# Performance work log

Hardware: AMD Instinct MI355X
Metric: run time of the kernel (lower is better)

## Reference

```python
import math
import jax, jax.numpy as jnp
import numpy as np

FS = 16000          # sample rate implied by undefined global `fs` in source
NFFT = 320          # win_len == frame_len
HOP = 160           # inc
C_SOUND = 340.0
ARRAY_DIS = 0.027


def _steering(F, n_ch, angle_deg):
    # h = conj(exp(-1j*2*pi*f_k * sensor * d * sin(theta)/c)) -> exp(+1j*...)
    f_k = np.arange(F) * (FS // NFFT)                      # integer bins * 50 Hz
    delay = np.arange(n_ch) * ARRAY_DIS * np.sin(angle_deg * np.pi / 180.0) / C_SOUND
    h = np.exp(1j * 2.0 * np.pi * f_k[:, None] * delay[None, :]).astype(np.complex64)
    return jnp.asarray(h)[..., None]                       # [F, C, 1]


def _stft(x, window):
    # x: [B, C, L] float32; torch.stft defaults: center=True, reflect pad
    pad = NFFT // 2
    xp = jnp.pad(x, ((0, 0), (0, 0), (pad, pad)), mode='reflect')
    T = 1 + (xp.shape[-1] - NFFT) // HOP
    idx = jnp.arange(T)[:, None] * HOP + jnp.arange(NFFT)[None, :]
    frames = xp[:, :, idx] * window                        # [B, C, T, NFFT]
    return jnp.fft.rfft(frames, axis=-1)                   # [B, C, T, F] complex64


def _istft(S):
    # S: [B, F, T] complex; torch.istft with default (rectangular) window
    frames = jnp.fft.irfft(jnp.moveaxis(S, 1, 2), n=NFFT, axis=-1)  # [B, T, NFFT]
    B, T, _ = frames.shape
    out_len = NFFT + HOP * (T - 1)
    idx = jnp.arange(T)[:, None] * HOP + jnp.arange(NFFT)[None, :]
    out = jnp.zeros((B, out_len), frames.dtype).at[:, idx].add(frames)
    wsum = jnp.zeros((out_len,), frames.dtype).at[idx.reshape(-1)].add(1.0)
    pad = NFFT // 2
    return (out / wsum)[:, pad:-pad]


def setup_inputs() -> dict:
    key = jax.random.key(0)
    B, L, C = 8, 160000, 4
    mc_wav = jax.random.normal(key, (B, L, C), dtype=jnp.float32)
    # torch.kaiser_window(320, periodic=True, beta=6)
    window = jnp.asarray(np.kaiser(NFFT + 1, 6.0)[:NFFT].astype(np.float32))
    return {"mc_wav": mc_wav, "window": window}


def reference(mc_wav, window):
    B, L, C = mc_wav.shape
    # pre-normalize: remove DC per channel, scale by per-batch global max-abs
    x = mc_wav - jnp.mean(mc_wav, axis=1, keepdims=True)
    x = x / jnp.max(jnp.abs(x), axis=(1, 2), keepdims=True)
    x = jnp.transpose(x, (0, 2, 1))                        # [B, C, L]

    S = _stft(x, window)                                   # [B, C, T, F]
    F = S.shape[-1]
    Xs = jnp.transpose(S, (2, 0, 3, 1))                    # [T, B, F, C] frames-first
    T = Xs.shape[0]

    h1 = _steering(F, C, -40.0)                            # [F, C, 1]
    h2 = _steering(F, C, 40.0)
    eye = jnp.eye(C, dtype=S.dtype)

    def beam(invR, h, X):
        num = jnp.einsum('bfcd,fdo->bfco', invR, h)        # invR @ h  [B,F,C,1]
        den = jnp.einsum('fco,bfco->bf', h.conj(), num)    # h^H invR h
        w = num[..., 0] / den[..., None]                   # [B, F, C]
        return jnp.einsum('bfc,bfc->bf', w.conj(), X)      # w^H X

    def step(RXX, inp):
        X, first = inp                                     # X: [B, F, C]
        outer = jnp.einsum('bfc,bfd->bfcd', X, X.conj())
        RXX = jnp.where(first, outer, 0.05 * RXX + 0.95 * outer)
        tr = jnp.trace(RXX, axis1=-2, axis2=-1)[..., None, None]
        invR = jnp.linalg.inv(RXX + (tr / C) * eye)        # diag-loaded inverse
        return RXX, (beam(invR, h1, X), beam(invR, h2, X))

    RXX0 = jnp.zeros((B, F, C, C), dtype=S.dtype)
    firsts = jnp.arange(T) == 0
    _, (s1, s2) = jax.lax.scan(step, RXX0, (Xs, firsts))

    S1 = jnp.transpose(s1, (1, 2, 0))                      # [B, F, T]
    S2 = jnp.transpose(s2, (1, 2, 0))
    return _istft(S1), _istft(S2)
```

## Files before the change

### kernel.cpp

```cpp
#include <hip/hip_runtime.h>
#include <hip/hip_bf16.h>
#include <math.h>

#define BB 8
#define LL 160000
#define CC 4
#define NFFT 320
#define HOP 160
#define FB 161
#define TT 1001
#define TP 1024
#define RBLK 128
#define PI_D 3.14159265358979323846
#define NPAD 160320

#define SCH 504
#define KWARM 4

#define GM 16016
#define KSEC 352
#define LDK 704
#define KT 11

typedef __attribute__((ext_vector_type(8))) short bf16x8;
typedef __attribute__((ext_vector_type(4))) float f32x4;

__device__ __forceinline__ void ldsdma16(const short* g, short* l){
    __builtin_amdgcn_global_load_lds((const __attribute__((address_space(1))) void*)g,
                                     (__attribute__((address_space(3))) void*)l, 16, 0, 0);
}

__device__ __forceinline__ float2 cmulf(float2 a, float2 b){
    return make_float2(a.x*b.x - a.y*b.y, a.x*b.y + a.y*b.x);
}
__device__ __forceinline__ float2 cmulcj(float2 a, float2 b){
    return make_float2(a.x*b.x + a.y*b.y, a.y*b.x - a.x*b.y);
}
__device__ __forceinline__ float2 cjmul(float2 a, float2 b){
    return make_float2(a.x*b.x + a.y*b.y, a.x*b.y - a.y*b.x);
}
__device__ __forceinline__ float2 csub(float2 a, float2 b){ return make_float2(a.x-b.x, a.y-b.y); }
__device__ __forceinline__ float2 cscale(float2 a, float s){ return make_float2(a.x*s, a.y*s); }
__device__ __forceinline__ float2 cdivf(float2 a, float2 b){
    float inv = 1.0f/(b.x*b.x + b.y*b.y);
    return make_float2((a.x*b.x + a.y*b.y)*inv, (a.y*b.x - a.x*b.y)*inv);
}
__device__ __forceinline__ short bf_hi(float v){
    __hip_bfloat16 h = __float2bfloat16(v);
    short s; __builtin_memcpy(&s, &h, 2); return s;
}
__device__ __forceinline__ short bf_lo(float v){
    __hip_bfloat16 h = __float2bfloat16(v);
    float r = v - __bfloat162float(h);
    __hip_bfloat16 l = __float2bfloat16(r);
    short s; __builtin_memcpy(&s, &l, 2); return s;
}

__global__ void k_gen(const float* __restrict__ win, float* __restrict__ htab,
                      short* __restrict__ Bts, short* __restrict__ Bt){
    int gid = blockIdx.x*256 + threadIdx.x;
    if (gid < 2*FB*CC){
        int i = gid;
        int c = i & 3;
        int k = (i >> 2) % FB;
        int m = i / (FB*CC);
        double coef = 2.0*PI_D*50.0*0.027*sin(40.0*PI_D/180.0)/340.0;
        double sgn = (m == 0) ? -1.0 : 1.0;
        double ph = sgn*coef*(double)k*(double)c;
        double s, c2;
        sincos(ph, &s, &c2);
        ((float2*)htab)[i] = make_float2((float)c2, (float)s);
        return;
    }
    gid -= 2*FB*CC;
    if (gid < 384*640){
        int col = gid / 640, kk = gid % 640;
        int n = (kk >= 320) ? kk - 320 : kk;
        int sec = (kk >= 320) ? 1 : 0;
        float v = 0.f;
        if (col < 2*FB){
            int k = col >> 1;
            double th = 2.0*PI_D*(double)k*(double)n/320.0;
            double s, co; sincos(th, &s, &co);
            double tw = (col & 1) ? -s : co;
            v = (float)((double)win[n]*tw);
        }
        Bts[gid] = sec ? bf_lo(v) : bf_hi(v);
        return;
    }
    gid -= 384*640;
    if (gid < NFFT*LDK){
        int n = gid / LDK, kk = gid % LDK;
        int sec = (kk >= KSEC) ? 1 : 0;
        int kk2 = kk - (sec ? KSEC : 0);
        float v = 0.f;
        if (kk2 < 2*FB){
            int bin = kk2 >> 1;
            double c = ((bin == 0 || bin == 160) ? 1.0 : 2.0) / 320.0;
            double th = 2.0*PI_D*(double)bin*(double)n/320.0;
            double s, co; sincos(th, &s, &co);
            v = (float)((kk2 & 1) ? -c*s : c*co);
        }
        Bt[(size_t)n*LDK + kk] = sec ? bf_lo(v) : bf_hi(v);
    }
}

__global__ __launch_bounds__(256) void k_stats1(const float* __restrict__ in, float* __restrict__ part){
    __shared__ float4 s4[256];
    __shared__ float4 mn4[256];
    __shared__ float4 mx4[256];
    int b = blockIdx.x / RBLK, chunk = blockIdx.x % RBLK;
    int tid = threadIdx.x;
    const float4* p = (const float4*)(in + (size_t)b*LL*CC);
    const int per = LL / RBLK;
    int start = chunk*per;
    float4 s  = make_float4(0.f,0.f,0.f,0.f);
    float4 mn = make_float4( 3.4e38f, 3.4e38f, 3.4e38f, 3.4e38f);
    float4 mx = make_float4(-3.4e38f,-3.4e38f,-3.4e38f,-3.4e38f);
    for (int i = start + tid; i < start + per; i += 256){
        float4 v = p[i];
        s.x += v.x; s.y += v.y; s.z += v.z; s.w += v.w;
        mn.x = fminf(mn.x, v.x); mn.y = fminf(mn.y, v.y); mn.z = fminf(mn.z, v.z); mn.w = fminf(mn.w, v.w);
        mx.x = fmaxf(mx.x, v.x); mx.y = fmaxf(mx.y, v.y); mx.z = fmaxf(mx.z, v.z); mx.w = fmaxf(mx.w, v.w);
    }
    s4[tid] = s; mn4[tid] = mn; mx4[tid] = mx;
    __syncthreads();
    for (int st = 128; st >= 1; st >>= 1){
        if (tid < st){
            float4 a = s4[tid], c = s4[tid+st];
            s4[tid] = make_float4(a.x+c.x, a.y+c.y, a.z+c.z, a.w+c.w);
            float4 d = mn4[tid], e = mn4[tid+st];
            mn4[tid] = make_float4(fminf(d.x,e.x), fminf(d.y,e.y), fminf(d.z,e.z), fminf(d.w,e.w));
            float4 f = mx4[tid], g = mx4[tid+st];
            mx4[tid] = make_float4(fmaxf(f.x,g.x), fmaxf(f.y,g.y), fmaxf(f.z,g.z), fmaxf(f.w,g.w));
        }
        __syncthreads();
    }
    if (tid == 0){
        float* dst = part + (size_t)(b*RBLK + chunk)*12;
        float4 a = s4[0], d = mn4[0], f = mx4[0];
        dst[0]=a.x; dst[1]=a.y; dst[2]=a.z; dst[3]=a.w;
        dst[4]=d.x; dst[5]=d.y; dst[6]=d.z; dst[7]=d.w;
        dst[8]=f.x; dst[9]=f.y; dst[10]=f.z; dst[11]=f.w;
    }
}

__global__ __launch_bounds__(128) void k_stats2(const float* __restrict__ part,
                                                float* __restrict__ mean, float* __restrict__ invmax){
    __shared__ float4 s4[128];
    __shared__ float4 mn4[128];
    __shared__ float4 mx4[128];
    int b = blockIdx.x, tid = threadIdx.x;
    const float* src = part + (size_t)(b*RBLK + tid)*12;
    s4[tid]  = make_float4(src[0], src[1], src[2], src[3]);
    mn4[tid] = make_float4(src[4], src[5], src[6], src[7]);
    mx4[tid] = make_float4(src[8], src[9], src[10], src[11]);
    __syncthreads();
    for (int st = 64; st >= 1; st >>= 1){
        if (tid < st){
            float4 a = s4[tid], c = s4[tid+st];
            s4[tid] = make_float4(a.x+c.x, a.y+c.y, a.z+c.z, a.w+c.w);
            float4 d = mn4[tid], e = mn4[tid+st];
            mn4[tid] = make_float4(fminf(d.x,e.x), fminf(d.y,e.y), fminf(d.z,e.z), fminf(d.w,e.w));
            float4 f = mx4[tid], g = mx4[tid+st];
            mx4[tid] = make_float4(fmaxf(f.x,g.x), fmaxf(f.y,g.y), fmaxf(f.z,g.z), fmaxf(f.w,g.w));
        }
        __syncthreads();
    }
    if (tid == 0){
        float4 sum = s4[0], mn = mn4[0], mx = mx4[0];
        float m0 = sum.x*(1.0f/LL), m1 = sum.y*(1.0f/LL), m2 = sum.z*(1.0f/LL), m3 = sum.w*(1.0f/LL);
        mean[b*4+0]=m0; mean[b*4+1]=m1; mean[b*4+2]=m2; mean[b*4+3]=m3;
        float a0 = fmaxf(mx.x - m0, m0 - mn.x);
        float a1 = fmaxf(mx.y - m1, m1 - mn.y);
        float a2 = fmaxf(mx.z - m2, m2 - mn.z);
        float a3 = fmaxf(mx.w - m3, m3 - mn.w);
        invmax[b] = 1.0f / fmaxf(fmaxf(a0, a1), fmaxf(a2, a3));
    }
}

__global__ __launch_bounds__(256) void k_anorm(const float* __restrict__ in,
        const float* __restrict__ mean, const float* __restrict__ invmax,
        short* __restrict__ Ahi, short* __restrict__ Alo){
    int gid = blockIdx.x*256 + threadIdx.x;
    if (gid >= BB*CC*(NPAD/8)) return;
    int p8 = gid % (NPAD/8);
    int bc = gid / (NPAD/8);
    int b = bc >> 2;
    float mc = mean[bc];
    float iv = invmax[b];
    const float* px = in + (size_t)b*LL*CC + (bc & 3);
    bf16x8 h8, l8;
    #pragma unroll
    for (int j = 0; j < 8; ++j){
        int p = p8*8 + j - 160;
        int m2 = p < 0 ? -p : (p >= LL ? 2*LL - 2 - p : p);
        float v = (px[(size_t)m2*CC] - mc) * iv;
        __hip_bfloat16 h = __float2bfloat16(v);
        float r = v - __bfloat162float(h);
        __hip_bfloat16 l = __float2bfloat16(r);
        short hs, ls; __builtin_memcpy(&hs, &h, 2); __builtin_memcpy(&ls, &l, 2);
        h8[j] = hs; l8[j] = ls;
    }
    size_t o = (size_t)bc*NPAD + (size_t)p8*8;
    *(bf16x8*)&Ahi[o] = h8;
    *(bf16x8*)&Alo[o] = l8;
}

__global__ __launch_bounds__(512, 4) void k_gstft(const short* __restrict__ Ahi, const short* __restrict__ Alo,
        const short* __restrict__ Bts, float* __restrict__ S){
    __shared__ short stage[32768];
    int tid = threadIdx.x;
    int row0 = blockIdx.x*128;
    int col0 = blockIdx.y*128;
    int b  = row0 >> 12;
    int t0 = (row0 & 4095) >> 2;
    int wave = tid >> 6, lane = tid & 63;
    int wm = wave >> 1, wn = wave & 1;
    int l15 = lane & 15, quad = lane >> 4;
    int rowS  = wave*16 + (lane >> 2);
    int chunk = (lane & 3) ^ ((lane >> 3) & 3);
    int tls = t0 + (rowS >> 2); if (tls >= TT) tls = TT - 1;
    size_t gao = (size_t)(b*4 + (rowS & 3))*NPAD + (size_t)tls*160 + chunk*8;
    const short* gAh = Ahi + gao;
    const short* gAl = Alo + gao;
    const short* gB  = Bts + (size_t)(col0 + rowS)*640 + chunk*8;
    short* lA = stage + wave*512;
    int sw  = (l15 >> 1) & 3;
    int c0r = (quad ^ sw) * 8;
    int ra0 = (wm*32 + l15)*32 + c0r;
    int rb0 = (wn*64 + l15)*32 + c0r;
    f32x4 c00 = {0.f,0.f,0.f,0.f}, c01 = c00, c02 = c00, c03 = c00;
    f32x4 c10 = c00, c11 = c00, c12 = c00, c13 = c00;

    #define STG(kt_, off_) do{ \
        ldsdma16(gAh + (kt_)*32,       lA + (off_));         \
        ldsdma16(gAl + (kt_)*32,       lA + (off_) + 4096);  \
        ldsdma16(gB  + (kt_)*32,       lA + (off_) + 8192);  \
        ldsdma16(gB  + (kt_)*32 + 320, lA + (off_) + 12288); \
    }while(0)

    STG(0, 0);
    STG(1, 16384);
    #pragma unroll
    for (int kt = 0; kt < 10; ++kt){
        int offc = (kt & 1) ? 16384 : 0;
        if (kt < 9) asm volatile("s_waitcnt vmcnt(4)" ::: "memory");
        else        asm volatile("s_waitcnt vmcnt(0)" ::: "memory");
        __builtin_amdgcn_s_barrier();
        bf16x8 a0h = *(bf16x8*)&stage[offc + ra0];
        bf16x8 a1h = *(bf16x8*)&stage[offc + ra0 + 512];
        bf16x8 a0l = *(bf16x8*)&stage[offc + 4096 + ra0];
        bf16x8 a1l = *(bf16x8*)&stage[offc + 4096 + ra0 + 512];
        bf16x8 b0h = *(bf16x8*)&stage[offc + 8192 + rb0];
        bf16x8 b1h = *(bf16x8*)&stage[offc + 8192 + rb0 + 512];
        bf16x8 b2h = *(bf16x8*)&stage[offc + 8192 + rb0 + 1024];
        bf16x8 b3h = *(bf16x8*)&stage[offc + 8192 + rb0 + 1536];
        bf16x8 b0l = *(bf16x8*)&stage[offc + 12288 + rb0];
        bf16x8 b1l = *(bf16x8*)&stage[offc + 12288 + rb0 + 512];
        bf16x8 b2l = *(bf16x8*)&stage[offc + 12288 + rb0 + 1024];
        bf16x8 b3l = *(bf16x8*)&stage[offc + 12288 + rb0 + 1536];
        asm volatile("s_waitcnt lgkmcnt(0)" ::: "memory");
        __builtin_amdgcn_sched_barrier(0);
        __builtin_amdgcn_s_barrier();
        if (kt < 8) STG(kt+2, offc);
        c00 = __builtin_amdgcn_mfma_f32_16x16x32_bf16(a0h, b0h, c00, 0, 0, 0);
        c01 = __builtin_amdgcn_mfma_f32_16x16x32_bf16(a0h, b1h, c01, 0, 0, 0);
        c02 = __builtin_amdgcn_mfma_f32_16x16x32_bf16(a0h, b2h, c02, 0, 0, 0);
        c03 = __builtin_amdgcn_mfma_f32_16x16x32_bf16(a0h, b3h, c03, 0, 0, 0);
        c10 = __builtin_amdgcn_mfma_f32_16x16x32_bf16(a1h, b0h, c10, 0, 0, 0);
        c11 = __builtin_amdgcn_mfma_f32_16x16x32_bf16(a1h, b1h, c11, 0, 0, 0);
        c12 = __builtin_amdgcn_mfma_f32_16x16x32_bf16(a1h, b2h, c12, 0, 0, 0);
        c13 = __builtin_amdgcn_mfma_f32_16x16x32_bf16(a1h, b3h, c13, 0, 0, 0);
        c00 = __builtin_amdgcn_mfma_f32_16x16x32_bf16(a0l, b0h, c00, 0, 0, 0);
        c01 = __builtin_amdgcn_mfma_f32_16x16x32_bf16(a0l, b1h, c01, 0, 0, 0);
        c02 = __builtin_amdgcn_mfma_f32_16x16x32_bf16(a0l, b2h, c02, 0, 0, 0);
        c03 = __builtin_amdgcn_mfma_f32_16x16x32_bf16(a0l, b3h, c03, 0, 0, 0);
        c10 = __builtin_amdgcn_mfma_f32_16x16x32_bf16(a1l, b0h, c10, 0, 0, 0);
        c11 = __builtin_amdgcn_mfma_f32_16x16x32_bf16(a1l, b1h, c11, 0, 0, 0);
        c12 = __builtin_amdgcn_mfma_f32_16x16x32_bf16(a1l, b2h, c12, 0, 0, 0);
        c13 = __builtin_amdgcn_mfma_f32_16x16x32_bf16(a1l, b3h, c13, 0, 0, 0);
        c00 = __builtin_amdgcn_mfma_f32_16x16x32_bf16(a0h, b0l, c00, 0, 0, 0);
        c01 = __builtin_amdgcn_mfma_f32_16x16x32_bf16(a0h, b1l, c01, 0, 0, 0);
        c02 = __builtin_amdgcn_mfma_f32_16x16x32_bf16(a0h, b2l, c02, 0, 0, 0);
        c03 = __builtin_amdgcn_mfma_f32_16x16x32_bf16(a0h, b3l, c03, 0, 0, 0);
        c10 = __builtin_amdgcn_mfma_f32_16x16x32_bf16(a1h, b0l, c10, 0, 0, 0);
        c11 = __builtin_amdgcn_mfma_f32_16x16x32_bf16(a1h, b1l, c11, 0, 0, 0);
        c12 = __builtin_amdgcn_mfma_f32_16x16x32_bf16(a1h, b2l, c12, 0, 0, 0);
        c13 = __builtin_amdgcn_mfma_f32_16x16x32_bf16(a1h, b3l, c13, 0, 0, 0);
    }
    #undef STG
    int tq  = t0 + wm*8 + quad;
    int kgb = (col0 >> 1) + wn*32 + (l15 >> 1);
    int h   = l15 & 1;
    float4* S4 = (float4*)S;
    #define EPI(cf, i_, j_) do{ \
        int t = tq + 4*(i_); \
        int kg = kgb + 8*(j_); \
        if (t < TT && kg < FB){ \
            float p0 = __shfl_xor(cf[0], 1); \
            float p1 = __shfl_xor(cf[1], 1); \
            float p2 = __shfl_xor(cf[2], 1); \
            float p3 = __shfl_xor(cf[3], 1); \
            float4 v = h ? make_float4(p2, cf[2], p3, cf[3]) \
                         : make_float4(cf[0], p0, cf[1], p1); \
            S4[((size_t)((b*FB + kg)*2 + h))*TT + t] = v; \
        } \
    }while(0)
    EPI(c00, 0, 0); EPI(c01, 0, 1); EPI(c02, 0, 2); EPI(c03, 0, 3);
    EPI(c10, 1, 0); EPI(c11, 1, 1); EPI(c12, 1, 2); EPI(c13, 1, 3);
    #undef EPI
}

#define UPD(first) do{ \
    float aa = (first) ? 0.f : 0.05f; float wg = (first) ? 1.f : 0.95f; \
    float y0x=wg*x0.x, y0y=wg*x0.y, y1x=wg*x1.x, y1y=wg*x1.y; \
    float y2x=wg*x2.x, y2y=wg*x2.y, y3x=wg*x3.x, y3y=wg*x3.y; \
    d0 = aa*d0 + y0x*x0.x + y0y*x0.y; \
    d1 = aa*d1 + y1x*x1.x + y1y*x1.y; \
    d2 = aa*d2 + y2x*x2.x + y2y*x2.y; \
    d3 = aa*d3 + y3x*x3.x + y3y*x3.y; \
    r10.x = aa*r10.x + y1x*x0.x + y1y*x0.y;  r10.y = aa*r10.y + y1y*x0.x - y1x*x0.y; \
    r20.x = aa*r20.x + y2x*x0.x + y2y*x0.y;  r20.y = aa*r20.y + y2y*x0.x - y2x*x0.y; \
    r30.x = aa*r30.x + y3x*x0.x + y3y*x0.y;  r30.y = aa*r30.y + y3y*x0.x - y3x*x0.y; \
    r21.x = aa*r21.x + y2x*x1.x + y2y*x1.y;  r21.y = aa*r21.y + y2y*x1.x - y2x*x1.y; \
    r31.x = aa*r31.x + y3x*x1.x + y3y*x1.y;  r31.y = aa*r31.y + y3y*x1.x - y3x*x1.y; \
    r32.x = aa*r32.x + y3x*x2.x + y3y*x2.y;  r32.y = aa*r32.y + y3y*x2.x - y3x*x2.y; \
}while(0)

__global__ __launch_bounds__(512) void k_scan(const float* __restrict__ S, const float* __restrict__ htab,
                      float* __restrict__ S1, float* __restrict__ S2){
    __shared__ float4 tile[1008];
    int bid = blockIdx.x;
    int half = bid & 1;
    int bf = bid >> 1;
    int f  = bf % FB;
    int tid = threadIdx.x;
    int tbase = half*SCH;
    int te  = tbase + SCH; if (te > TT) te = TT;
    int nst = 2*(te - tbase);
    const float4* P0 = (const float4*)S + (size_t)(bf*2)*TT;
    const float4* P1 = P0 + TT;
    for (int i = tid; i < nst; i += 512){
        int tt = tbase + (i >> 1);
        tile[i ^ ((i>>4)&7)] = (i & 1) ? P1[tt] : P0[tt];
    }
    __syncthreads();
    float2 out1, out2;
    int t0 = tbase + tid;
    bool act = (tid < SCH) && (t0 < TT);
    if (act){
        const float2* hp = (const float2*)htab;
        float2 ha0 = hp[f*4+0], ha1 = hp[f*4+1], ha2 = hp[f*4+2], ha3 = hp[f*4+3];
        float2 hb0 = hp[(FB+f)*4+0], hb1 = hp[(FB+f)*4+1], hb2 = hp[(FB+f)*4+2], hb3 = hp[(FB+f)*4+3];
        float d0=0,d1=0,d2=0,d3=0;
        float2 r10={0,0}, r20={0,0}, r30={0,0}, r21={0,0}, r31={0,0}, r32={0,0};
        int ts = t0 - KWARM; if (ts < 0) ts = 0;
        for (int tau = ts; tau < t0; ++tau){
            float4 v0, v1;
            if (tau >= tbase){
                int i0 = 2*(tau - tbase);
                v0 = tile[i0 ^ ((i0>>4)&7)];
                v1 = tile[(i0+1) ^ ((i0>>4)&7)];
            } else {
                v0 = P0[tau];
                v1 = P1[tau];
            }
            float2 x0 = make_float2(v0.x, v0.y), x1 = make_float2(v0.z, v0.w);
            float2 x2 = make_float2(v1.x, v1.y), x3 = make_float2(v1.z, v1.w);
            UPD(tau == 0);
        }
        {
            int t = t0;
            int i0 = 2*(t - tbase);
            float4 v0 = tile[i0 ^ ((i0>>4)&7)];
            float4 v1 = tile[(i0+1) ^ ((i0>>4)&7)];
            float2 x0 = make_float2(v0.x, v0.y), x1 = make_float2(v0.z, v0.w);
            float2 x2 = make_float2(v1.x, v1.y), x3 = make_float2(v1.z, v1.w);
            UPD(t == 0);
            float trc = d0 + d1 + d2 + d3;
            float lam = trc * 0.25f;
            float e0 = d0 + lam, e1 = d1 + lam, e2 = d2 + lam, e3 = d3 + lam;
            float detP = e0*e1 - (r10.x*r10.x + r10.y*r10.y);
            float2 w00 = csub(cscale(r20, e1), cmulf(r10, r21));
            float2 w01 = csub(cscale(r30, e1), cmulf(r10, r31));
            float2 w10 = csub(cscale(r21, e0), cjmul(r10, r20));
            float2 w11 = csub(cscale(r31, e0), cjmul(r10, r30));
            float2 va = cjmul(r30, w00), vb = cjmul(r31, w10);
            float2 V10 = make_float2(va.x + vb.x, -(va.y + vb.y));
            float reV00 = r20.x*w00.x + r20.y*w00.y + r21.x*w10.x + r21.y*w10.y;
            float reV11 = r30.x*w01.x + r30.y*w01.y + r31.x*w11.x + r31.y*w11.y;
            float t00 = detP*e2 - reV00;
            float t11 = detP*e3 - reV11;
            float2 t10 = csub(cscale(r32, detP), V10);
            float detT = t00*t11 - (t10.x*t10.x + t10.y*t10.y);
            #pragma unroll
            for (int m = 0; m < 2; ++m){
                float2 h0 = m ? hb0 : ha0;
                float2 h1 = m ? hb1 : ha1;
                float2 h2 = m ? hb2 : ha2;
                float2 h3 = m ? hb3 : ha3;
                float2 g0 = csub(cscale(h0, e1), cjmul(r10, h1));
                float2 g1 = csub(cscale(h1, e0), cmulf(r10, h0));
                float2 ta = cmulf(r20, g0), tb = cmulf(r21, g1);
                float2 hh0 = make_float2(detP*h2.x - ta.x - tb.x, detP*h2.y - ta.y - tb.y);
                ta = cmulf(r30, g0); tb = cmulf(r31, g1);
                float2 hh1 = make_float2(detP*h3.x - ta.x - tb.x, detP*h3.y - ta.y - tb.y);
                float2 y20 = csub(cscale(hh0, t11), cjmul(t10, hh1));
                float2 y21 = csub(cscale(hh1, t00), cmulf(t10, hh0));
                float2 u20 = cscale(y20, detP), u21 = cscale(y21, detP);
                ta = cmulcj(y20, r20); tb = cmulcj(y21, r30);
                float2 q0 = make_float2(detT*h0.x - ta.x - tb.x, detT*h0.y - ta.y - tb.y);
                ta = cmulcj(y20, r21); tb = cmulcj(y21, r31);
                float2 q1 = make_float2(detT*h1.x - ta.x - tb.x, detT*h1.y - ta.y - tb.y);
                float2 u10 = csub(cscale(q0, e1), cjmul(r10, q1));
                float2 u11 = csub(cscale(q1, e0), cmulf(r10, q0));
                float2 den = cjmul(h0, u10), tmp;
                tmp = cjmul(h1, u11); den.x += tmp.x; den.y += tmp.y;
                tmp = cjmul(h2, u20); den.x += tmp.x; den.y += tmp.y;
                tmp = cjmul(h3, u21); den.x += tmp.x; den.y += tmp.y;
                float2 num = cjmul(u10, x0);
                tmp = cjmul(u11, x1); num.x += tmp.x; num.y += tmp.y;
                tmp = cjmul(u20, x2); num.x += tmp.x; num.y += tmp.y;
                tmp = cjmul(u21, x3); num.x += tmp.x; num.y += tmp.y;
                float2 s = cdivf(num, make_float2(den.x, -den.y));
                if (m) out2 = s; else out1 = s;
            }
        }
    }
    __syncthreads();
    float2* o1 = (float2*)tile;
    float2* o2 = ((float2*)tile) + 528;
    if (act){
        int lt = t0 - tbase;
        int iw = lt ^ ((lt>>3)&7);
        o1[iw] = out1;
        o2[iw] = out2;
    }
    __syncthreads();
    int nout = te - tbase;
    float2* S1g = (float2*)S1 + (size_t)bf*TT + tbase;
    float2* S2g = (float2*)S2 + (size_t)bf*TT + tbase;
    for (int i = tid; i < nout; i += 512){
        int ir = i ^ ((i>>3)&7);
        S1g[i] = o1[ir];
        S2g[i] = o2[ir];
    }
}

__global__ __launch_bounds__(256) void k_pack(const float* __restrict__ S1, const float* __restrict__ S2,
                                              short* __restrict__ A){
    __shared__ short tile[32*708];
    int bid = blockIdx.x;
    int tb = bid & 31, rb = bid >> 5;
    int t0 = tb*32;
    int beam = rb >> 3, b = rb & 7;
    const float2* Sp = (const float2*)(beam ? S2 : S1) + (size_t)b*FB*TT;
    int tid = threadIdx.x;
    for (int idx = tid; idx < 32*176; idx += 256){
        int bin = idx >> 5, tq = idx & 31;
        int t = t0 + tq;
        float2 s = make_float2(0.f, 0.f);
        if (bin < FB && t < TT) s = Sp[(size_t)bin*TT + t];
        int c0 = 2*bin;
        tile[tq*708 + c0]            = bf_hi(s.x);
        tile[tq*708 + c0 + 1]        = bf_hi(s.y);
        tile[tq*708 + KSEC + c0]     = bf_lo(s.x);
        tile[tq*708 + KSEC + c0 + 1] = bf_lo(s.y);
    }
    __syncthreads();
    for (int idx = tid; idx < 32*176; idx += 256){
        int tq = idx / 176, k4 = idx % 176;
        int t = t0 + tq;
        if (t < TT)
            *(short4*)&A[(size_t)(rb*TT + t)*LDK + k4*4] = *(short4*)&tile[tq*708 + k4*4];
    }
}

__global__ __launch_bounds__(512, 4) void k_gemm(const short* __restrict__ A, const short* __restrict__ Bt,
                                                 float* __restrict__ C){
    __shared__ short sb2[16384];
    int tid = threadIdx.x;
    int row0 = blockIdx.x * 128;
    int col0 = blockIdx.y * 128;
    int wave = tid >> 6, lane = tid & 63;
    int wm = wave >> 1, wn = wave & 1;
    int l15 = lane & 15, quad = lane >> 4;
    int rowS  = wave*16 + (lane >> 2);
    int chunk = (lane & 3) ^ ((lane >> 3) & 3);
    int grS = row0 + rowS; if (grS >= GM) grS = GM - 1;
    int grB = col0 + rowS; if (grB >= NFFT) grB = NFFT - 1;
    const short* gA = A  + (size_t)grS*LDK + chunk*8;
    const short* gB = Bt + (size_t)grB*LDK + chunk*8;
    short* lA = sb2 + wave*512;
    int sw  = (l15 >> 1) & 3;
    int c0r = (quad ^ sw) * 8;
    int ra0 = (wm*32 + l15)*32 + c0r;
    int rb0 = (wn*64 + l15)*32 + c0r;
    f32x4 c00 = {0.f,0.f,0.f,0.f}, c01 = c00, c02 = c00, c03 = c00;
    f32x4 c10 = c00, c11 = c00, c12 = c00, c13 = c00;

    #define KOF(s_, ka_, kb_) { int sg_ = ((s_) >= 22) ? 2 : ((s_) >= 11) ? 1 : 0; \
        int kt_ = (s_) - sg_*11; \
        ka_ = ((sg_ == 1) ? KSEC : 0) + kt_*32; \
        kb_ = ((sg_ == 2) ? KSEC : 0) + kt_*32; }
    #define STG2(s_, off_) do{ int ka_, kb_; KOF(s_, ka_, kb_); \
        ldsdma16(gA + ka_, lA + (off_));        \
        ldsdma16(gB + kb_, lA + (off_) + 4096); \
    }while(0)

    STG2(0, 0);
    STG2(1, 8192);
    #pragma unroll
    for (int s = 0; s < 33; ++s){
        int offc = (s & 1) ? 8192 : 0;
        if (s < 32) asm volatile("s_waitcnt vmcnt(2)" ::: "memory");
        else        asm volatile("s_waitcnt vmcnt(0)" ::: "memory");
        __builtin_amdgcn_s_barrier();
        bf16x8 a0 = *(bf16x8*)&sb2[offc + ra0];
        bf16x8 a1 = *(bf16x8*)&sb2[offc + ra0 + 512];
        bf16x8 b0 = *(bf16x8*)&sb2[offc + 4096 + rb0];
        bf16x8 b1 = *(bf16x8*)&sb2[offc + 4096 + rb0 + 512];
        bf16x8 b2 = *(bf16x8*)&sb2[offc + 4096 + rb0 + 1024];
        bf16x8 b3 = *(bf16x8*)&sb2[offc + 4096 + rb0 + 1536];
        asm volatile("s_waitcnt lgkmcnt(0)" ::: "memory");
        __builtin_amdgcn_sched_barrier(0);
        __builtin_amdgcn_s_barrier();
        if (s < 31) STG2(s+2, offc);
        c00 = __builtin_amdgcn_mfma_f32_16x16x32_bf16(a0, b0, c00, 0, 0, 0);
        c01 = __builtin_amdgcn_mfma_f32_16x16x32_bf16(a0, b1, c01, 0, 0, 0);
        c02 = __builtin_amdgcn_mfma_f32_16x16x32_bf16(a0, b2, c02, 0, 0, 0);
        c03 = __builtin_amdgcn_mfma_f32_16x16x32_bf16(a0, b3, c03, 0, 0, 0);
        c10 = __builtin_amdgcn_mfma_f32_16x16x32_bf16(a1, b0, c10, 0, 0, 0);
        c11 = __builtin_amdgcn_mfma_f32_16x16x32_bf16(a1, b1, c11, 0, 0, 0);
        c12 = __builtin_amdgcn_mfma_f32_16x16x32_bf16(a1, b2, c12, 0, 0, 0);
        c13 = __builtin_amdgcn_mfma_f32_16x16x32_bf16(a1, b3, c13, 0, 0, 0);
    }
    #undef STG2
    #undef KOF
    #pragma unroll
    for (int r = 0; r < 4; ++r){
        int orow0 = row0 + wm*32 + quad*4 + r;
        int oc = col0 + wn*64 + l15;
        if (orow0 < GM){
            if (oc      < NFFT) C[(size_t)orow0*NFFT + oc]      = c00[r];
            if (oc + 16 < NFFT) C[(size_t)orow0*NFFT + oc + 16] = c01[r];
            if (oc + 32 < NFFT) C[(size_t)orow0*NFFT + oc + 32] = c02[r];
            if (oc + 48 < NFFT) C[(size_t)orow0*NFFT + oc + 48] = c03[r];
        }
        if (orow0 + 16 < GM){
            if (oc      < NFFT) C[(size_t)(orow0+16)*NFFT + oc]      = c10[r];
            if (oc + 16 < NFFT) C[(size_t)(orow0+16)*NFFT + oc + 16] = c11[r];
            if (oc + 32 < NFFT) C[(size_t)(orow0+16)*NFFT + oc + 32] = c12[r];
            if (oc + 48 < NFFT) C[(size_t)(orow0+16)*NFFT + oc + 48] = c13[r];
        }
    }
}

__global__ __launch_bounds__(256) void k_ola(const float* __restrict__ frames, float* __restrict__ out){
    int gid = blockIdx.x*256 + threadIdx.x;
    if (gid >= 2*BB*(LL/4)) return;
    int o4 = (gid % (LL/4))*4;
    int rb = gid / (LL/4);
    int i  = o4 + HOP;
    int t1 = i / HOP;
    int r  = i - t1*HOP;
    const float4* fb = (const float4*)(frames + (size_t)rb*TT*NFFT);
    float4 a = fb[(t1*NFFT + r) >> 2];
    float4 b = fb[((t1-1)*NFFT + r + HOP) >> 2];
    ((float4*)out)[gid] = make_float4(0.5f*(a.x+b.x), 0.5f*(a.y+b.y), 0.5f*(a.z+b.z), 0.5f*(a.w+b.w));
}

extern "C" void kernel_launch(void* const* d_in, const int* in_sizes, int n_in,
                              void* d_out, int out_size, void* d_ws, size_t ws_size,
                              hipStream_t stream){
    const float* in  = (const float*)d_in[0];
    const float* win = (const float*)d_in[1];
    float* ws = (float*)d_ws;
    float* mean   = ws;
    float* invmax = ws + 32;
    float* htab   = ws + 48;
    float* S1     = ws + 3072;
    size_t nS1 = (size_t)2*BB*FB*TT;
    float* S2 = S1 + nS1;
    float* S  = S2 + nS1;
    float* part = S1;
    short* Ahi = (short*)S1;
    short* Alo = Ahi + (size_t)BB*CC*NPAD;
    short* Bts = (short*)d_out;
    short* Bt  = (short*)((float*)d_out + 131072);
    short* A  = (short*)S;
    float* frames = S1;

    int ngen = 2*FB*CC + 384*640 + NFFT*LDK;
    k_gen<<<dim3((ngen + 255)/256), dim3(256), 0, stream>>>(win, htab, Bts, Bt);
    k_stats1<<<dim3(BB*RBLK), dim3(256), 0, stream>>>(in, part);
    k_stats2<<<dim3(BB), dim3(128), 0, stream>>>(part, mean, invmax);
    k_anorm<<<dim3((BB*CC*(NPAD/8) + 255)/256), dim3(256), 0, stream>>>(in, mean, invmax, Ahi, Alo);
    k_gstft<<<dim3(BB*TP*CC/128, 3), dim3(512), 0, stream>>>(Ahi, Alo, Bts, S);
    k_scan<<<dim3(2*BB*FB), dim3(512), 0, stream>>>(S, htab, S1, S2);
    k_pack<<<dim3(512), dim3(256), 0, stream>>>(S1, S2, A);
    k_gemm<<<dim3((GM + 127)/128, (NFFT + 127)/128), dim3(512), 0, stream>>>(A, Bt, frames);
    k_ola<<<dim3((2*BB*(LL/4) + 255)/256), dim3(256), 0, stream>>>(frames, (float*)d_out);
}
```

Baseline: 209.5 us.

## Vectorize normalize loads, simplify scan warmup and stores, skip dead GEMM waves

k_anorm now handles all four channels per thread, reading one float4 per sample instead of four strided scalar loads, and writes four channel rows of hi/lo bf16. k_scan unrolls the fixed-length warmup with a specialized update that has no first-step branch, and writes outputs straight to global memory instead of staging them through shared memory behind two barriers. k_gemm skips LDS loads, MFMAs and stores for waves whose column range falls entirely past NFFT in the last column tile. The direct scan stores may be less coalesced, and bf_hi/bf_lo helpers are assumed to exist in the hidden code.

```diff
diff --git a/kernel.cpp b/kernel.cpp
--- a/kernel.cpp
+++ b/kernel.cpp
@@ -183,28 +183,30 @@
         const float* __restrict__ mean, const float* __restrict__ invmax,
         short* __restrict__ Ahi, short* __restrict__ Alo){
     int gid = blockIdx.x*256 + threadIdx.x;
-    if (gid >= BB*CC*(NPAD/8)) return;
+    if (gid >= BB*(NPAD/8)) return;
     int p8 = gid % (NPAD/8);
-    int bc = gid / (NPAD/8);
-    int b = bc >> 2;
-    float mc = mean[bc];
+    int b  = gid / (NPAD/8);
+    float4 mc = *(const float4*)&mean[b*4];
     float iv = invmax[b];
-    const float* px = in + (size_t)b*LL*CC + (bc & 3);
-    bf16x8 h8, l8;
+    const float4* px = (const float4*)(in + (size_t)b*LL*CC);
+    bf16x8 h0{}, h1{}, h2{}, h3{}, l0{}, l1{}, l2{}, l3{};
     #pragma unroll
     for (int j = 0; j < 8; ++j){
         int p = p8*8 + j - 160;
         int m2 = p < 0 ? -p : (p >= LL ? 2*LL - 2 - p : p);
-        float v = (px[(size_t)m2*CC] - mc) * iv;
-        __hip_bfloat16 h = __float2bfloat16(v);
-        float r = v - __bfloat162float(h);
-        __hip_bfloat16 l = __float2bfloat16(r);
-        short hs, ls; __builtin_memcpy(&hs, &h, 2); __builtin_memcpy(&ls, &l, 2);
-        h8[j] = hs; l8[j] = ls;
-    }
-    size_t o = (size_t)bc*NPAD + (size_t)p8*8;
-    *(bf16x8*)&Ahi[o] = h8;
-    *(bf16x8*)&Alo[o] = l8;
+        float4 v = px[m2];
+        float v0 = (v.x - mc.x)*iv, v1 = (v.y - mc.y)*iv;
+        float v2 = (v.z - mc.z)*iv, v3 = (v.w - mc.w)*iv;
+        h0[j] = bf_hi(v0); l0[j] = bf_lo(v0);
+        h1[j] = bf_hi(v1); l1[j] = bf_lo(v1);
+        h2[j] = bf_hi(v2); l2[j] = bf_lo(v2);
+        h3[j] = bf_hi(v3); l3[j] = bf_lo(v3);
+    }
+    size_t o = (size_t)(b*4)*NPAD + (size_t)p8*8;
+    *(bf16x8*)&Ahi[o]          = h0;  *(bf16x8*)&Alo[o]          = l0;
+    *(bf16x8*)&Ahi[o +   NPAD] = h1;  *(bf16x8*)&Alo[o +   NPAD] = l1;
+    *(bf16x8*)&Ahi[o + 2*NPAD] = h2;  *(bf16x8*)&Alo[o + 2*NPAD] = l2;
+    *(bf16x8*)&Ahi[o + 3*NPAD] = h3;  *(bf16x8*)&Alo[o + 3*NPAD] = l3;
 }
 
 __global__ __launch_bounds__(512, 4) void k_gstft(const short* __restrict__ Ahi, const short* __restrict__ Alo,
@@ -328,6 +330,19 @@
     r32.x = aa*r32.x + y3x*x2.x + y3y*x2.y;  r32.y = aa*r32.y + y3y*x2.x - y3x*x2.y; \
 }while(0)
 
+#define UPDQ do{ \
+    d0 = 0.05f*d0 + x0.x*x0.x + x0.y*x0.y; \
+    d1 = 0.05f*d1 + x1.x*x1.x + x1.y*x1.y; \
+    d2 = 0.05f*d2 + x2.x*x2.x + x2.y*x2.y; \
+    d3 = 0.05f*d3 + x3.x*x3.x + x3.y*x3.y; \
+    r10.x = 0.05f*r10.x + x1.x*x0.x + x1.y*x0.y;  r10.y = 0.05f*r10.y + x1.y*x0.x - x1.x*x0.y; \
+    r20.x = 0.05f*r20.x + x2.x*x0.x + x2.y*x0.y;  r20.y = 0.05f*r20.y + x2.y*x0.x - x2.x*x0.y; \
+    r30.x = 0.05f*r30.x + x3.x*x0.x + x3.y*x0.y;  r30.y = 0.05f*r30.y + x3.y*x0.x - x3.x*x0.y; \
+    r21.x = 0.05f*r21.x + x2.x*x1.x + x2.y*x1.y;  r21.y = 0.05f*r21.y + x2.y*x1.x - x2.x*x1.y; \
+    r31.x = 0.05f*r31.x + x3.x*x1.x + x3.y*x1.y;  r31.y = 0.05f*r31.y + x3.y*x1.x - x3.x*x1.y; \
+    r32.x = 0.05f*r32.x + x3.x*x2.x + x3.y*x2.y;  r32.y = 0.05f*r32.y + x3.y*x2.x - x3.x*x2.y; \
+}while(0)
+
 __global__ __launch_bounds__(512) void k_scan(const float* __restrict__ S, const float* __restrict__ htab,
                       float* __restrict__ S1, float* __restrict__ S2){
     __shared__ float4 tile[1008];
@@ -346,7 +361,6 @@
         tile[i ^ ((i>>4)&7)] = (i & 1) ? P1[tt] : P0[tt];
     }
     __syncthreads();
-    float2 out1, out2;
     int t0 = tbase + tid;
     bool act = (tid < SCH) && (t0 < TT);
     if (act){
@@ -355,29 +369,22 @@
         float2 hb0 = hp[(FB+f)*4+0], hb1 = hp[(FB+f)*4+1], hb2 = hp[(FB+f)*4+2], hb3 = hp[(FB+f)*4+3];
         float d0=0,d1=0,d2=0,d3=0;
         float2 r10={0,0}, r20={0,0}, r30={0,0}, r21={0,0}, r31={0,0}, r32={0,0};
-        int ts = t0 - KWARM; if (ts < 0) ts = 0;
-        for (int tau = ts; tau < t0; ++tau){
-            float4 v0, v1;
-            if (tau >= tbase){
-                int i0 = 2*(tau - tbase);
-                v0 = tile[i0 ^ ((i0>>4)&7)];
-                v1 = tile[(i0+1) ^ ((i0>>4)&7)];
-            } else {
-                v0 = P0[tau];
-                v1 = P1[tau];
-            }
-            float2 x0 = make_float2(v0.x, v0.y), x1 = make_float2(v0.z, v0.w);
-            float2 x2 = make_float2(v1.x, v1.y), x3 = make_float2(v1.z, v1.w);
-            UPD(tau == 0);
-        }
+        float2 x0, x1, x2, x3;
+        #define LOADX(tau_) do{ float4 v0_, v1_; \
+            if ((tau_) >= tbase){ int i0_ = 2*((tau_) - tbase); \
+                v0_ = tile[i0_ ^ ((i0_>>4)&7)]; v1_ = tile[(i0_+1) ^ ((i0_>>4)&7)]; } \
+            else { v0_ = P0[tau_]; v1_ = P1[tau_]; } \
+            x0 = make_float2(v0_.x, v0_.y); x1 = make_float2(v0_.z, v0_.w); \
+            x2 = make_float2(v1_.x, v1_.y); x3 = make_float2(v1_.z, v1_.w); \
+        }while(0)
+        if (t0 >= KWARM + 1){
+            #pragma unroll
+            for (int u = 0; u <= KWARM; ++u){ LOADX(t0 - KWARM + u); UPDQ; }
+        } else {
+            for (int tau = 0; tau <= t0; ++tau){ LOADX(tau); UPD(tau == 0); }
+        }
+        #undef LOADX
         {
-            int t = t0;
-            int i0 = 2*(t - tbase);
-            float4 v0 = tile[i0 ^ ((i0>>4)&7)];
-            float4 v1 = tile[(i0+1) ^ ((i0>>4)&7)];
-            float2 x0 = make_float2(v0.x, v0.y), x1 = make_float2(v0.z, v0.w);
-            float2 x2 = make_float2(v1.x, v1.y), x3 = make_float2(v1.z, v1.w);
-            UPD(t == 0);
             float trc = d0 + d1 + d2 + d3;
             float lam = trc * 0.25f;
             float e0 = d0 + lam, e1 = d1 + lam, e2 = d2 + lam, e3 = d3 + lam;
@@ -394,6 +401,8 @@
             float t11 = detP*e3 - reV11;
             float2 t10 = csub(cscale(r32, detP), V10);
             float detT = t00*t11 - (t10.x*t10.x + t10.y*t10.y);
+            float2* S1g = (float2*)S1 + (size_t)bf*TT;
+            float2* S2g = (float2*)S2 + (size_t)bf*TT;
             #pragma unroll
             for (int m = 0; m < 2; ++m){
                 float2 h0 = m ? hb0 : ha0;
@@ -424,27 +433,9 @@
                 tmp = cjmul(u20, x2); num.x += tmp.x; num.y += tmp.y;
                 tmp = cjmul(u21, x3); num.x += tmp.x; num.y += tmp.y;
                 float2 s = cdivf(num, make_float2(den.x, -den.y));
-                if (m) out2 = s; else out1 = s;
+                if (m) S2g[t0] = s; else S1g[t0] = s;
             }
         }
-    }
-    __syncthreads();
-    float2* o1 = (float2*)tile;
-    float2* o2 = ((float2*)tile) + 528;
-    if (act){
-        int lt = t0 - tbase;
-        int iw = lt ^ ((lt>>3)&7);
-        o1[iw] = out1;
-        o2[iw] = out2;
-    }
-    __syncthreads();
-    int nout = te - tbase;
-    float2* S1g = (float2*)S1 + (size_t)bf*TT + tbase;
-    float2* S2g = (float2*)S2 + (size_t)bf*TT + tbase;
-    for (int i = tid; i < nout; i += 512){
-        int ir = i ^ ((i>>3)&7);
-        S1g[i] = o1[ir];
-        S2g[i] = o2[ir];
     }
 }
 
@@ -486,6 +477,7 @@
     int wave = tid >> 6, lane = tid & 63;
     int wm = wave >> 1, wn = wave & 1;
     int l15 = lane & 15, quad = lane >> 4;
+    bool wlive = (col0 + wn*64) < NFFT;
     int rowS  = wave*16 + (lane >> 2);
     int chunk = (lane & 3) ^ ((lane >> 3) & 3);
     int grS = row0 + rowS; if (grS >= GM) grS = GM - 1;
@@ -517,42 +509,49 @@
         if (s < 32) asm volatile("s_waitcnt vmcnt(2)" ::: "memory");
         else        asm volatile("s_waitcnt vmcnt(0)" ::: "memory");
         __builtin_amdgcn_s_barrier();
-        bf16x8 a0 = *(bf16x8*)&sb2[offc + ra0];
-        bf16x8 a1 = *(bf16x8*)&sb2[offc + ra0 + 512];
-        bf16x8 b0 = *(bf16x8*)&sb2[offc + 4096 + rb0];
-        bf16x8 b1 = *(bf16x8*)&sb2[offc + 4096 + rb0 + 512];
-        bf16x8 b2 = *(bf16x8*)&sb2[offc + 4096 + rb0 + 1024];
-        bf16x8 b3 = *(bf16x8*)&sb2[offc + 4096 + rb0 + 1536];
-        asm volatile("s_waitcnt lgkmcnt(0)" ::: "memory");
-        __builtin_amdgcn_sched_barrier(0);
+        bf16x8 a0{}, a1{}, b0{}, b1{}, b2{}, b3{};
+        if (wlive){
+            a0 = *(bf16x8*)&sb2[offc + ra0];
+            a1 = *(bf16x8*)&sb2[offc + ra0 + 512];
+            b0 = *(bf16x8*)&sb2[offc + 4096 + rb0];
+            b1 = *(bf16x8*)&sb2[offc + 4096 + rb0 + 512];
+            b2 = *(bf16x8*)&sb2[offc + 4096 + rb0 + 1024];
+            b3 = *(bf16x8*)&sb2[offc + 4096 + rb0 + 1536];
+            asm volatile("s_waitcnt lgkmcnt(0)" ::: "memory");
+            __builtin_amdgcn_sched_barrier(0);
+        }
         __builtin_amdgcn_s_barrier();
         if (s < 31) STG2(s+2, offc);
-        c00 = __builtin_amdgcn_mfma_f32_16x16x32_bf16(a0, b0, c00, 0, 0, 0);
-        c01 = __builtin_amdgcn_mfma_f32_16x16x32_bf16(a0, b1, c01, 0, 0, 0);
-        c02 = __builtin_amdgcn_mfma_f32_16x16x32_bf16(a0, b2, c02, 0, 0, 0);
-        c03 = __builtin_amdgcn_mfma_f32_16x16x32_bf16(a0, b3, c03, 0, 0, 0);
-        c10 = __builtin_amdgcn_mfma_f32_16x16x32_bf16(a1, b0, c10, 0, 0, 0);
-        c11 = __builtin_amdgcn_mfma_f32_16x16x32_bf16(a1, b1, c11, 0, 0, 0);
-        c12 = __builtin_amdgcn_mfma_f32_16x16x32_bf16(a1, b2, c12, 0, 0, 0);
-        c13 = __builtin_amdgcn_mfma_f32_16x16x32_bf16(a1, b3, c13, 0, 0, 0);
+        if (wlive){
+            c00 = __builtin_amdgcn_mfma_f32_16x16x32_bf16(a0, b0, c00, 0, 0, 0);
+            c01 = __builtin_amdgcn_mfma_f32_16x16x32_bf16(a0, b1, c01, 0, 0, 0);
+            c02 = __builtin_amdgcn_mfma_f32_16x16x32_bf16(a0, b2, c02, 0, 0, 0);
+            c03 = __builtin_amdgcn_mfma_f32_16x16x32_bf16(a0, b3, c03, 0, 0, 0);
+            c10 = __builtin_amdgcn_mfma_f32_16x16x32_bf16(a1, b0, c10, 0, 0, 0);
+            c11 = __builtin_amdgcn_mfma_f32_16x16x32_bf16(a1, b1, c11, 0, 0, 0);
+            c12 = __builtin_amdgcn_mfma_f32_16x16x32_bf16(a1, b2, c12, 0, 0, 0);
+            c13 = __builtin_amdgcn_mfma_f32_16x16x32_bf16(a1, b3, c13, 0, 0, 0);
+        }
     }
     #undef STG2
     #undef KOF
-    #pragma unroll
-    for (int r = 0; r < 4; ++r){
-        int orow0 = row0 + wm*32 + quad*4 + r;
-        int oc = col0 + wn*64 + l15;
-        if (orow0 < GM){
-            if (oc      < NFFT) C[(size_t)orow0*NFFT + oc]      = c00[r];
-            if (oc + 16 < NFFT) C[(size_t)orow0*NFFT + oc + 16] = c01[r];
-            if (oc + 32 < NFFT) C[(size_t)orow0*NFFT + oc + 32] = c02[r];
-            if (oc + 48 < NFFT) C[(size_t)orow0*NFFT + oc + 48] = c03[r];
-        }
-        if (orow0 + 16 < GM){
-            if (oc      < NFFT) C[(size_t)(orow0+16)*NFFT + oc]      = c10[r];
-            if (oc + 16 < NFFT) C[(size_t)(orow0+16)*NFFT + oc + 16] = c11[r];
-            if (oc + 32 < NFFT) C[(size_t)(orow0+16)*NFFT + oc + 32] = c12[r];
-            if (oc + 48 < NFFT) C[(size_t)(orow0+16)*NFFT + oc + 48] = c13[r];
+    if (wlive){
+        #pragma unroll
+        for (int r = 0; r < 4; ++r){
+            int orow0 = row0 + wm*32 + quad*4 + r;
+            int oc = col0 + wn*64 + l15;
+            if (orow0 < GM){
+                if (oc      < NFFT) C[(size_t)orow0*NFFT + oc]      = c00[r];
+                if (oc + 16 < NFFT) C[(size_t)orow0*NFFT + oc + 16] = c01[r];
+                if (oc + 32 < NFFT) C[(size_t)orow0*NFFT + oc + 32] = c02[r];
+                if (oc + 48 < NFFT) C[(size_t)orow0*NFFT + oc + 48] = c03[r];
+            }
+            if (orow0 + 16 < GM){
+                if (oc      < NFFT) C[(size_t)(orow0+16)*NFFT + oc]      = c10[r];
+                if (oc + 16 < NFFT) C[(size_t)(orow0+16)*NFFT + oc + 16] = c11[r];
+                if (oc + 32 < NFFT) C[(size_t)(orow0+16)*NFFT + oc + 32] = c12[r];
+                if (oc + 48 < NFFT) C[(size_t)(orow0+16)*NFFT + oc + 48] = c13[r];
+            }
         }
     }
 }
@@ -596,7 +595,7 @@
     k_gen<<<dim3((ngen + 255)/256), dim3(256), 0, stream>>>(win, htab, Bts, Bt);
     k_stats1<<<dim3(BB*RBLK), dim3(256), 0, stream>>>(in, part);
     k_stats2<<<dim3(BB), dim3(128), 0, stream>>>(part, mean, invmax);
-    k_anorm<<<dim3((BB*CC*(NPAD/8) + 255)/256), dim3(256), 0, stream>>>(in, mean, invmax, Ahi, Alo);
+    k_anorm<<<dim3((BB*(NPAD/8) + 255)/256), dim3(256), 0, stream>>>(in, mean, invmax, Ahi, Alo);
     k_gstft<<<dim3(BB*TP*CC/128, 3), dim3(512), 0, stream>>>(Ahi, Alo, Bts, S);
     k_scan<<<dim3(2*BB*FB), dim3(512), 0, stream>>>(S, htab, S1, S2);
     k_pack<<<dim3(512), dim3(256), 0, stream>>>(S1, S2, A);
```

Result: faster. 194.8 us (-7.0%).
